# Performance work log

Hardware: AMD Instinct MI355X
Metric: run time of the kernel (lower is better)

## Reference

```python
import jax, jax.numpy as jnp
import numpy as np

H = 6      # n_attention_heads
BLK = 64


def adder1x1(x2d, w):
    """AdderNet 1x1 'convolution': Y[co, n] = -sum_ci |x2d[ci, n] - w[co, ci]|.
    Processed in output-channel blocks to bound the abs-diff intermediate.
    x2d: [Ci, N], w: [Co, Ci] -> [Co, N]
    """
    co, ci = w.shape
    wb = w.reshape(co // BLK, BLK, ci)
    def f(wblk):  # wblk: [BLK, Ci] -> [BLK, N]
        return -jnp.sum(jnp.abs(x2d[None, :, :] - wblk[:, :, None]), axis=1)
    return jax.lax.map(f, wb).reshape(co, -1)


def layernorm_all(y, w, b, eps=1e-5):
    # nn.LayerNorm([E, B, S]) applied to [1, E, B, S]: normalize over ALL of E,B,S
    mu = jnp.mean(y)
    var = jnp.mean((y - mu) ** 2)
    return (y - mu) * jax.lax.rsqrt(var + eps) * w + b


def layernorm_last(y, w, b, eps=1e-5):
    mu = jnp.mean(y, axis=-1, keepdims=True)
    var = jnp.mean((y - mu) ** 2, axis=-1, keepdims=True)
    return (y - mu) * jax.lax.rsqrt(var + eps) * w + b


def setup_inputs() -> dict:
    key = jax.random.key(0)
    ks = jax.random.split(key, 14)
    B, S, E = 8, 197, 384
    inp = {
        "x": jax.random.normal(ks[0], (B, S, E), jnp.float32),
        "wq": jax.random.normal(ks[1], (E, E), jnp.float32) * 0.05,
        "wk": jax.random.normal(ks[2], (E, E), jnp.float32) * 0.05,
        "wv": jax.random.normal(ks[3], (E, E), jnp.float32) * 0.05,
        "qln_w": 1.0 + 0.02 * jax.random.normal(ks[4], (E, B, S), jnp.float32),
        "qln_b": 0.02 * jax.random.normal(ks[5], (E, B, S), jnp.float32),
        "kln_w": 1.0 + 0.02 * jax.random.normal(ks[6], (E, B, S), jnp.float32),
        "kln_b": 0.02 * jax.random.normal(ks[7], (E, B, S), jnp.float32),
        "vln_w": 1.0 + 0.02 * jax.random.normal(ks[8], (E, B, S), jnp.float32),
        "vln_b": 0.02 * jax.random.normal(ks[9], (E, B, S), jnp.float32),
        "oln_w": 1.0 + 0.02 * jax.random.normal(ks[10], (E,), jnp.float32),
        "oln_b": 0.02 * jax.random.normal(ks[11], (E,), jnp.float32),
        "fc_w": jax.random.normal(ks[12], (E, E), jnp.float32) * 0.05,
        "fc_b": 0.02 * jax.random.normal(ks[13], (E,), jnp.float32),
    }
    return inp


def reference(x, wq, wk, wv, qln_w, qln_b, kln_w, kln_b, vln_w, vln_b,
              oln_w, oln_b, fc_w, fc_b):
    B, S, E = x.shape
    D = E // H
    scale = (2.0 * D * (1.0 - 2.0 / np.pi)) ** (-0.5)

    # torch: x.reshape(1, E, B, S) on contiguous [B,S,E] is a flat-buffer reshape
    x2d = x.reshape(E, B * S)  # [Ci, N]

    def proj(w, lw, lb):
        y = adder1x1(x2d, w).reshape(E, B, S)          # adder2d 1x1, bias=False
        y = layernorm_all(y, lw, lb)                    # LN over [E,B,S]
        y = y.reshape(B, S, H, D)                       # flat reshape (as torch)
        y = jnp.swapaxes(y, 1, 2)                       # [B,H,S,D]
        return y.reshape(B * H, S, D)

    q = proj(wq, qln_w, qln_b)
    k = proj(wk, kln_w, kln_b)
    v = proj(wv, vln_w, vln_b)

    att = jnp.einsum('bsd,btd->bst', q, k) * scale      # [B*H, S, S]
    att = jax.nn.softmax(att, axis=-1) + jnp.eye(S, dtype=x.dtype)
    o = jnp.einsum('bst,btd->bsd', att, v)              # [B*H, S, D]

    o = jnp.swapaxes(o.reshape(B, H, S, D), 1, 2).reshape(B, S, E)
    o = layernorm_last(o, oln_w, oln_b)
    return o @ fc_w.T + fc_b
```

## Files before the change

kernel.cpp:

```cpp
#include <hip/hip_runtime.h>
#include <math.h>

#ifndef M_PI
#define M_PI 3.14159265358979323846
#endif

#define B_ 8
#define S_ 197
#define E_ 384
#define H_ 6
#define D_ 64
#define N_ (B_*S_)
#define EN ((size_t)E_*N_)
#define NBLK_N 7
#define NBLK_ADD (NBLK_N*48)
#define NBLK_LN 591

__global__ __launch_bounds__(256) void k_adder(
    const float* __restrict__ x,
    const float* __restrict__ wq, const float* __restrict__ wk,
    const float* __restrict__ wv,
    float* __restrict__ Y, float* __restrict__ partials)
{
  const int p = blockIdx.z;
  const float* __restrict__ w = (p == 0) ? wq : (p == 1) ? wk : wv;
  const int co0 = blockIdx.y * 8;
  const int n = blockIdx.x * 256 + threadIdx.x;
  const bool nok = (n < N_);
  const int nc = nok ? n : 0;

  const float* __restrict__ xp = x + nc;
  const float* __restrict__ wp = w + (size_t)co0 * E_;

  float acc[8];
  #pragma unroll
  for (int r = 0; r < 8; ++r) acc[r] = 0.f;

  float xbA[8], xbB[8];
  #pragma unroll
  for (int k = 0; k < 8; ++k) xbA[k] = xp[(size_t)k * N_];

  #pragma unroll 1
  for (int c0 = 0; c0 < E_; c0 += 16) {
    #pragma unroll
    for (int k = 0; k < 8; ++k) xbB[k] = xp[(size_t)(c0 + 8 + k) * N_];
    #pragma unroll
    for (int r = 0; r < 8; ++r) {
      const float* wr = wp + (size_t)r * E_ + c0;
      #pragma unroll
      for (int k = 0; k < 8; ++k)
        acc[r] += fabsf(xbA[k] - wr[k]);
    }
    if (c0 + 16 < E_) {
      #pragma unroll
      for (int k = 0; k < 8; ++k) xbA[k] = xp[(size_t)(c0 + 16 + k) * N_];
    }
    #pragma unroll
    for (int r = 0; r < 8; ++r) {
      const float* wr = wp + (size_t)r * E_ + c0 + 8;
      #pragma unroll
      for (int k = 0; k < 8; ++k)
        acc[r] += fabsf(xbB[k] - wr[k]);
    }
  }

  float* Yp = Y + (size_t)p * EN;
  if (nok) {
    #pragma unroll
    for (int r = 0; r < 8; ++r)
      Yp[(size_t)(co0 + r) * N_ + n] = -acc[r];
  }

  float s1 = 0.f, s2 = 0.f;
  if (nok) {
    #pragma unroll
    for (int r = 0; r < 8; ++r) {
      s1 += -acc[r];
      s2 += acc[r] * acc[r];
    }
  }
  #pragma unroll
  for (int off = 32; off > 0; off >>= 1) {
    s1 += __shfl_down(s1, off);
    s2 += __shfl_down(s2, off);
  }
  __shared__ float red[8];
  const int tid = threadIdx.x;
  int wid = tid >> 6, lane = tid & 63;
  if (lane == 0) { red[wid * 2] = s1; red[wid * 2 + 1] = s2; }
  __syncthreads();
  if (tid == 0) {
    float t1 = red[0] + red[2] + red[4] + red[6];
    float t2 = red[1] + red[3] + red[5] + red[7];
    int blk = blockIdx.y * NBLK_N + blockIdx.x;
    partials[((size_t)p * NBLK_ADD + blk) * 2 + 0] = t1;
    partials[((size_t)p * NBLK_ADD + blk) * 2 + 1] = t2;
  }
}

__global__ __launch_bounds__(256) void k_stats(
    const float* __restrict__ partials, float* __restrict__ stats)
{
  const int p = blockIdx.x;
  const int tid = threadIdx.x;
  float s1 = 0.f, s2 = 0.f;
  for (int i = tid; i < NBLK_ADD; i += 256) {
    s1 += partials[((size_t)p * NBLK_ADD + i) * 2 + 0];
    s2 += partials[((size_t)p * NBLK_ADD + i) * 2 + 1];
  }
  #pragma unroll
  for (int off = 32; off > 0; off >>= 1) {
    s1 += __shfl_down(s1, off);
    s2 += __shfl_down(s2, off);
  }
  __shared__ float red[8];
  int wid = tid >> 6, lane = tid & 63;
  if (lane == 0) { red[wid * 2] = s1; red[wid * 2 + 1] = s2; }
  __syncthreads();
  if (tid == 0) {
    float S1 = red[0] + red[2] + red[4] + red[6];
    float S2 = red[1] + red[3] + red[5] + red[7];
    float mean = S1 / (float)EN;
    float var = S2 / (float)EN - mean * mean;
    stats[p * 2 + 0] = mean;
    stats[p * 2 + 1] = rsqrtf(var + 1e-5f);
  }
}

__global__ __launch_bounds__(256) void k_lnall(
    const float* __restrict__ Y, float* __restrict__ Z,
    const float* __restrict__ stats,
    const float* __restrict__ w0, const float* __restrict__ b0,
    const float* __restrict__ w1, const float* __restrict__ b1,
    const float* __restrict__ w2, const float* __restrict__ b2)
{
  const int p = blockIdx.y;
  const float* __restrict__ w = (p == 0) ? w0 : (p == 1) ? w1 : w2;
  const float* __restrict__ b = (p == 0) ? b0 : (p == 1) ? b1 : b2;
  const float mean = stats[p * 2 + 0];
  const float rstd = stats[p * 2 + 1];
  size_t i = ((size_t)blockIdx.x * 256 + threadIdx.x) * 4;
  const float* Yp = Y + (size_t)p * EN;
  float* Zp = Z + (size_t)p * EN;
  float4 y = *(const float4*)(Yp + i);
  float4 wv = *(const float4*)(w + i);
  float4 bv = *(const float4*)(b + i);
  float4 zv;
  zv.x = (y.x - mean) * rstd * wv.x + bv.x;
  zv.y = (y.y - mean) * rstd * wv.y + bv.y;
  zv.z = (y.z - mean) * rstd * wv.z + bv.z;
  zv.w = (y.w - mean) * rstd * wv.w + bv.w;
  *(float4*)(Zp + i) = zv;
}

__global__ __launch_bounds__(256) void k_attn(
    const float* __restrict__ zq, const float* __restrict__ zk,
    const float* __restrict__ zv, float* __restrict__ obuf, float scale)
{
  const int bh = blockIdx.x, b = bh / H_, h = bh % H_;
  const int s0 = blockIdx.y * 32;

  __shared__ float Qs[64][36];
  __shared__ float KVs[64][68];
  __shared__ float Ps[32][200];
  __shared__ float linv[32];

  const int tid = threadIdx.x;
  const int tx = tid & 15, ty = tid >> 4;

  #pragma unroll
  for (int it = 0; it < 2; ++it) {
    int idx = tid + it * 256;
    int sl = idx >> 4, c4 = (idx & 15) * 4;
    int s = s0 + sl;
    float4 v = make_float4(0.f, 0.f, 0.f, 0.f);
    if (s < S_) v = *(const float4*)(zq + (size_t)(b * S_ + s) * E_ + h * D_ + c4);
    Qs[c4 + 0][sl] = v.x; Qs[c4 + 1][sl] = v.y;
    Qs[c4 + 2][sl] = v.z; Qs[c4 + 3][sl] = v.w;
  }

  float accS[4][2][4];
  #pragma unroll
  for (int tt = 0; tt < 4; ++tt)
    #pragma unroll
    for (int r = 0; r < 2; ++r)
      #pragma unroll
      for (int j = 0; j < 4; ++j) accS[tt][r][j] = 0.f;

  #pragma unroll
  for (int tt = 0; tt < 4; ++tt) {
    __syncthreads();
    #pragma unroll
    for (int it = 0; it < 4; ++it) {
      int idx = tid + it * 256;
      int tl = idx >> 4, c4 = (idx & 15) * 4;
      int t = tt * 64 + tl;
      float4 u = make_float4(0.f, 0.f, 0.f, 0.f);
      if (t < S_) u = *(const float4*)(zk + (size_t)(b * S_ + t) * E_ + h * D_ + c4);
      KVs[c4 + 0][tl] = u.x; KVs[c4 + 1][tl] = u.y;
      KVs[c4 + 2][tl] = u.z; KVs[c4 + 3][tl] = u.w;
    }
    __syncthreads();
    #pragma unroll 8
    for (int d = 0; d < 64; ++d) {
      float2 q2 = *(const float2*)(&Qs[d][2 * ty]);
      float4 k4 = *(const float4*)(&KVs[d][tx * 4]);
      float ka[4] = {k4.x, k4.y, k4.z, k4.w};
      #pragma unroll
      for (int j = 0; j < 4; ++j) {
        accS[tt][0][j] += q2.x * ka[j];
        accS[tt][1][j] += q2.y * ka[j];
      }
    }
  }

  float mr0 = -1e30f, mr1 = -1e30f;
  #pragma unroll
  for (int tt = 0; tt < 4; ++tt)
    #pragma unroll
    for (int j = 0; j < 4; ++j) {
      int t = tt * 64 + tx * 4 + j;
      float v0 = (t < S_) ? accS[tt][0][j] * scale : -1e30f;
      float v1 = (t < S_) ? accS[tt][1][j] * scale : -1e30f;
      accS[tt][0][j] = v0; accS[tt][1][j] = v1;
      mr0 = fmaxf(mr0, v0); mr1 = fmaxf(mr1, v1);
    }
  #pragma unroll
  for (int off = 1; off < 16; off <<= 1) {
    mr0 = fmaxf(mr0, __shfl_xor(mr0, off));
    mr1 = fmaxf(mr1, __shfl_xor(mr1, off));
  }
  float sr0 = 0.f, sr1 = 0.f;
  #pragma unroll
  for (int tt = 0; tt < 4; ++tt)
    #pragma unroll
    for (int j = 0; j < 4; ++j) {
      float p0 = __expf(accS[tt][0][j] - mr0);
      float p1 = __expf(accS[tt][1][j] - mr1);
      accS[tt][0][j] = p0; accS[tt][1][j] = p1;
      sr0 += p0; sr1 += p1;
    }
  #pragma unroll
  for (int off = 1; off < 16; off <<= 1) {
    sr0 += __shfl_xor(sr0, off);
    sr1 += __shfl_xor(sr1, off);
  }
  if (tx == 0) { linv[2 * ty] = 1.f / sr0; linv[2 * ty + 1] = 1.f / sr1; }
  #pragma unroll
  for (int tt = 0; tt < 4; ++tt) {
    int t4 = tt * 64 + tx * 4;
    if (t4 < 200) {
      *(float4*)(&Ps[2 * ty][t4]) =
          make_float4(accS[tt][0][0], accS[tt][0][1], accS[tt][0][2], accS[tt][0][3]);
      *(float4*)(&Ps[2 * ty + 1][t4]) =
          make_float4(accS[tt][1][0], accS[tt][1][1], accS[tt][1][2], accS[tt][1][3]);
    }
  }

  float accO[2][4];
  #pragma unroll
  for (int r = 0; r < 2; ++r)
    #pragma unroll
    for (int j = 0; j < 4; ++j) accO[r][j] = 0.f;

  #pragma unroll
  for (int tt = 0; tt < 4; ++tt) {
    __syncthreads();
    #pragma unroll
    for (int it = 0; it < 4; ++it) {
      int idx = tid + it * 256;
      int tl = idx >> 4, c4 = (idx & 15) * 4;
      int t = tt * 64 + tl;
      float4 u = make_float4(0.f, 0.f, 0.f, 0.f);
      if (t < S_) u = *(const float4*)(zv + (size_t)(b * S_ + t) * E_ + h * D_ + c4);
      *(float4*)(&KVs[tl][c4]) = u;
    }
    __syncthreads();
    const int tmax = (tt < 3) ? 64 : 8;
    #pragma unroll 8
    for (int tl = 0; tl < tmax; ++tl) {
      float p0 = Ps[2 * ty][tt * 64 + tl];
      float p1 = Ps[2 * ty + 1][tt * 64 + tl];
      float4 v4 = *(const float4*)(&KVs[tl][tx * 4]);
      float va[4] = {v4.x, v4.y, v4.z, v4.w};
      #pragma unroll
      for (int j = 0; j < 4; ++j) {
        accO[0][j] += p0 * va[j];
        accO[1][j] += p1 * va[j];
      }
    }
  }

  #pragma unroll
  for (int r = 0; r < 2; ++r) {
    int s = s0 + 2 * ty + r;
    if (s < S_) {
      float inv = linv[2 * ty + r];
      float4 vs = *(const float4*)(zv + (size_t)(b * S_ + s) * E_ + h * D_ + tx * 4);
      float4 o;
      o.x = accO[r][0] * inv + vs.x;
      o.y = accO[r][1] * inv + vs.y;
      o.z = accO[r][2] * inv + vs.z;
      o.w = accO[r][3] * inv + vs.w;
      *(float4*)(obuf + (size_t)(b * S_ + s) * E_ + h * D_ + tx * 4) = o;
    }
  }
}

__global__ __launch_bounds__(256) void k_lnlast(
    const float* __restrict__ obuf,
    const float* __restrict__ lw, const float* __restrict__ lb,
    float* __restrict__ oln)
{
  const int row = blockIdx.x * 4 + (threadIdx.x >> 6);
  const int lane = threadIdx.x & 63;
  const float* base = obuf + (size_t)row * E_;
  float v[6];
  float s1 = 0.f;
  #pragma unroll
  for (int j = 0; j < 6; ++j) { v[j] = base[lane + 64 * j]; s1 += v[j]; }
  #pragma unroll
  for (int off = 32; off > 0; off >>= 1) s1 += __shfl_xor(s1, off);
  float mean = s1 * (1.f / E_);
  float s2 = 0.f;
  #pragma unroll
  for (int j = 0; j < 6; ++j) { float d = v[j] - mean; s2 += d * d; }
  #pragma unroll
  for (int off = 32; off > 0; off >>= 1) s2 += __shfl_xor(s2, off);
  float rstd = rsqrtf(s2 * (1.f / E_) + 1e-5f);
  float* ob = oln + (size_t)row * E_;
  #pragma unroll
  for (int j = 0; j < 6; ++j) {
    int e = lane + 64 * j;
    ob[e] = (v[j] - mean) * rstd * lw[e] + lb[e];
  }
}

__global__ __launch_bounds__(256) void k_fc(
    const float* __restrict__ oln, const float* __restrict__ fcw,
    const float* __restrict__ fcb, float* __restrict__ out)
{
  const int j0 = blockIdx.x * 64, n0 = blockIdx.y * 32;
  __shared__ float Xs[16][36];
  __shared__ float Ws[16][68];
  const int tid = threadIdx.x;
  const int tx = tid & 15, ty = tid >> 4;
  float acc[4][2];
  #pragma unroll
  for (int i = 0; i < 4; ++i) { acc[i][0] = 0.f; acc[i][1] = 0.f; }

  for (int e0 = 0; e0 < E_; e0 += 16) {
    {
      int nl = tid >> 3, e2 = (tid & 7) * 2;
      int n = n0 + nl;
      float2 v = make_float2(0.f, 0.f);
      if (n < N_) v = *(const float2*)(oln + (size_t)n * E_ + e0 + e2);
      Xs[e2 + 0][nl] = v.x; Xs[e2 + 1][nl] = v.y;
      int jl = tid >> 2, c4 = (tid & 3) * 4;
      float4 u = *(const float4*)(fcw + (size_t)(j0 + jl) * E_ + e0 + c4);
      Ws[c4 + 0][jl] = u.x; Ws[c4 + 1][jl] = u.y;
      Ws[c4 + 2][jl] = u.z; Ws[c4 + 3][jl] = u.w;
    }
    __syncthreads();
    #pragma unroll
    for (int cc = 0; cc < 16; ++cc) {
      float2 x2 = *(const float2*)(&Xs[cc][tx * 2]);
      float4 w4 = *(const float4*)(&Ws[cc][ty * 4]);
      float xa[2] = {x2.x, x2.y};
      float wa[4] = {w4.x, w4.y, w4.z, w4.w};
      #pragma unroll
      for (int i = 0; i < 4; ++i) {
        acc[i][0] += wa[i] * xa[0];
        acc[i][1] += wa[i] * xa[1];
      }
    }
    __syncthreads();
  }
  const int jc = j0 + ty * 4;
  float4 bv = *(const float4*)(fcb + jc);
  #pragma unroll
  for (int jn = 0; jn < 2; ++jn) {
    int n = n0 + tx * 2 + jn;
    if (n < N_) {
      float4 o;
      o.x = acc[0][jn] + bv.x;
      o.y = acc[1][jn] + bv.y;
      o.z = acc[2][jn] + bv.z;
      o.w = acc[3][jn] + bv.w;
      *(float4*)(out + (size_t)n * E_ + jc) = o;
    }
  }
}

extern "C" void kernel_launch(void* const* d_in, const int* in_sizes, int n_in,
                              void* d_out, int out_size, void* d_ws, size_t ws_size,
                              hipStream_t stream)
{
  const float* x   = (const float*)d_in[0];
  const float* wq  = (const float*)d_in[1];
  const float* wk  = (const float*)d_in[2];
  const float* wv  = (const float*)d_in[3];
  const float* qw  = (const float*)d_in[4];
  const float* qb  = (const float*)d_in[5];
  const float* kw  = (const float*)d_in[6];
  const float* kb  = (const float*)d_in[7];
  const float* vw  = (const float*)d_in[8];
  const float* vb  = (const float*)d_in[9];
  const float* ow  = (const float*)d_in[10];
  const float* obp = (const float*)d_in[11];
  const float* fcw = (const float*)d_in[12];
  const float* fcb = (const float*)d_in[13];
  float* out = (float*)d_out;
  float* ws  = (float*)d_ws;

  float* Y     = ws;
  float* Z     = ws + 3 * EN;
  float* obuf  = ws + 0 * EN;
  float* oln   = ws + 1 * EN;
  float* part  = ws + 6 * EN;
  float* stats = part + 3 * NBLK_ADD * 2;

  const float scale = (float)pow(2.0 * D_ * (1.0 - 2.0 / M_PI), -0.5);

  k_adder<<<dim3(NBLK_N, 48, 3), 256, 0, stream>>>(x, wq, wk, wv, Y, part);
  k_stats<<<dim3(3), 256, 0, stream>>>(part, stats);
  k_lnall<<<dim3(NBLK_LN, 3), 256, 0, stream>>>(Y, Z, stats, qw, qb, kw, kb, vw, vb);
  const float* zq = Z;
  const float* zk = Z + EN;
  const float* zv = Z + 2 * EN;
  k_attn<<<dim3(48, 7), 256, 0, stream>>>(zq, zk, zv, obuf, scale);
  k_lnlast<<<dim3(394), 256, 0, stream>>>(obuf, ow, obp, oln);
  k_fc<<<dim3(6, 50), 256, 0, stream>>>(oln, fcw, fcb, out);
}
```

Baseline: 117.6 us.

## Shrink per-block tiles in adder and attention kernels to raise block counts

The adder kernel now has each block compute 6 output channels instead of 8, so the grid's y dimension grows from 48 to 64. Its x-row prefetch goes from two to four 8-wide register buffers per 32-channel step. The attention kernel now gives each block 16 query rows instead of 32, with one row per thread group, raising its grid from 7 to 13 blocks per head, and Q is stored row-major in shared memory. The aim is more blocks for better occupancy and load balance across CUs, at the cost of reloading K/V tiles for twice as many attention blocks and more x-buffer registers in the adder.

```diff
diff --git a/kernel.cpp b/kernel.cpp
--- a/kernel.cpp
+++ b/kernel.cpp
@@ -13,7 +13,8 @@
 #define N_ (B_*S_)
 #define EN ((size_t)E_*N_)
 #define NBLK_N 7
-#define NBLK_ADD (NBLK_N*48)
+#define NBLK_CO 64
+#define NBLK_ADD (NBLK_N*NBLK_CO)
 #define NBLK_LN 591
 
 __global__ __launch_bounds__(256) void k_adder(
@@ -24,7 +25,7 @@
 {
   const int p = blockIdx.z;
   const float* __restrict__ w = (p == 0) ? wq : (p == 1) ? wk : wv;
-  const int co0 = blockIdx.y * 8;
+  const int co0 = blockIdx.y * 6;
   const int n = blockIdx.x * 256 + threadIdx.x;
   const bool nok = (n < N_);
   const int nc = nok ? n : 0;
@@ -32,49 +33,75 @@
   const float* __restrict__ xp = x + nc;
   const float* __restrict__ wp = w + (size_t)co0 * E_;
 
-  float acc[8];
-  #pragma unroll
-  for (int r = 0; r < 8; ++r) acc[r] = 0.f;
-
-  float xbA[8], xbB[8];
-  #pragma unroll
-  for (int k = 0; k < 8; ++k) xbA[k] = xp[(size_t)k * N_];
+  float acc[6];
+  #pragma unroll
+  for (int r = 0; r < 6; ++r) acc[r] = 0.f;
+
+  float xb0[8], xb1[8], xb2[8], xb3[8];
+  #pragma unroll
+  for (int k = 0; k < 8; ++k) {
+    xb0[k] = xp[(size_t)(k +  0) * N_];
+    xb1[k] = xp[(size_t)(k +  8) * N_];
+    xb2[k] = xp[(size_t)(k + 16) * N_];
+    xb3[k] = xp[(size_t)(k + 24) * N_];
+  }
 
   #pragma unroll 1
-  for (int c0 = 0; c0 < E_; c0 += 16) {
-    #pragma unroll
-    for (int k = 0; k < 8; ++k) xbB[k] = xp[(size_t)(c0 + 8 + k) * N_];
-    #pragma unroll
-    for (int r = 0; r < 8; ++r) {
+  for (int c0 = 0; c0 < E_; c0 += 32) {
+    const bool more = (c0 + 32) < E_;
+    #pragma unroll
+    for (int r = 0; r < 6; ++r) {
       const float* wr = wp + (size_t)r * E_ + c0;
       #pragma unroll
-      for (int k = 0; k < 8; ++k)
-        acc[r] += fabsf(xbA[k] - wr[k]);
-    }
-    if (c0 + 16 < E_) {
-      #pragma unroll
-      for (int k = 0; k < 8; ++k) xbA[k] = xp[(size_t)(c0 + 16 + k) * N_];
-    }
-    #pragma unroll
-    for (int r = 0; r < 8; ++r) {
+      for (int k = 0; k < 8; ++k) acc[r] += fabsf(xb0[k] - wr[k]);
+    }
+    if (more) {
+      #pragma unroll
+      for (int k = 0; k < 8; ++k) xb0[k] = xp[(size_t)(c0 + 32 + k) * N_];
+    }
+    #pragma unroll
+    for (int r = 0; r < 6; ++r) {
       const float* wr = wp + (size_t)r * E_ + c0 + 8;
       #pragma unroll
-      for (int k = 0; k < 8; ++k)
-        acc[r] += fabsf(xbB[k] - wr[k]);
+      for (int k = 0; k < 8; ++k) acc[r] += fabsf(xb1[k] - wr[k]);
+    }
+    if (more) {
+      #pragma unroll
+      for (int k = 0; k < 8; ++k) xb1[k] = xp[(size_t)(c0 + 40 + k) * N_];
+    }
+    #pragma unroll
+    for (int r = 0; r < 6; ++r) {
+      const float* wr = wp + (size_t)r * E_ + c0 + 16;
+      #pragma unroll
+      for (int k = 0; k < 8; ++k) acc[r] += fabsf(xb2[k] - wr[k]);
+    }
+    if (more) {
+      #pragma unroll
+      for (int k = 0; k < 8; ++k) xb2[k] = xp[(size_t)(c0 + 48 + k) * N_];
+    }
+    #pragma unroll
+    for (int r = 0; r < 6; ++r) {
+      const float* wr = wp + (size_t)r * E_ + c0 + 24;
+      #pragma unroll
+      for (int k = 0; k < 8; ++k) acc[r] += fabsf(xb3[k] - wr[k]);
+    }
+    if (more) {
+      #pragma unroll
+      for (int k = 0; k < 8; ++k) xb3[k] = xp[(size_t)(c0 + 56 + k) * N_];
     }
   }
 
   float* Yp = Y + (size_t)p * EN;
   if (nok) {
     #pragma unroll
-    for (int r = 0; r < 8; ++r)
+    for (int r = 0; r < 6; ++r)
       Yp[(size_t)(co0 + r) * N_ + n] = -acc[r];
   }
 
   float s1 = 0.f, s2 = 0.f;
   if (nok) {
     #pragma unroll
-    for (int r = 0; r < 8; ++r) {
+    for (int r = 0; r < 6; ++r) {
       s1 += -acc[r];
       s2 += acc[r] * acc[r];
     }
@@ -158,34 +185,30 @@
     const float* __restrict__ zv, float* __restrict__ obuf, float scale)
 {
   const int bh = blockIdx.x, b = bh / H_, h = bh % H_;
-  const int s0 = blockIdx.y * 32;
-
-  __shared__ float Qs[64][36];
+  const int s0 = blockIdx.y * 16;
+
+  __shared__ float Qs[16][68];
   __shared__ float KVs[64][68];
-  __shared__ float Ps[32][200];
-  __shared__ float linv[32];
+  __shared__ float Ps[16][200];
+  __shared__ float linv[16];
 
   const int tid = threadIdx.x;
-  const int tx = tid & 15, ty = tid >> 4;
-
-  #pragma unroll
-  for (int it = 0; it < 2; ++it) {
-    int idx = tid + it * 256;
-    int sl = idx >> 4, c4 = (idx & 15) * 4;
+  const int tx = tid & 15;
+  const int ty = tid >> 4;
+
+  {
+    int sl = tid >> 4, c4 = (tid & 15) * 4;
     int s = s0 + sl;
     float4 v = make_float4(0.f, 0.f, 0.f, 0.f);
     if (s < S_) v = *(const float4*)(zq + (size_t)(b * S_ + s) * E_ + h * D_ + c4);
-    Qs[c4 + 0][sl] = v.x; Qs[c4 + 1][sl] = v.y;
-    Qs[c4 + 2][sl] = v.z; Qs[c4 + 3][sl] = v.w;
-  }
-
-  float accS[4][2][4];
+    *(float4*)(&Qs[sl][c4]) = v;
+  }
+
+  float accS[4][4];
   #pragma unroll
   for (int tt = 0; tt < 4; ++tt)
     #pragma unroll
-    for (int r = 0; r < 2; ++r)
-      #pragma unroll
-      for (int j = 0; j < 4; ++j) accS[tt][r][j] = 0.f;
+    for (int j = 0; j < 4; ++j) accS[tt][j] = 0.f;
 
   #pragma unroll
   for (int tt = 0; tt < 4; ++tt) {
@@ -201,68 +224,54 @@
       KVs[c4 + 2][tl] = u.z; KVs[c4 + 3][tl] = u.w;
     }
     __syncthreads();
-    #pragma unroll 8
-    for (int d = 0; d < 64; ++d) {
-      float2 q2 = *(const float2*)(&Qs[d][2 * ty]);
-      float4 k4 = *(const float4*)(&KVs[d][tx * 4]);
-      float ka[4] = {k4.x, k4.y, k4.z, k4.w};
-      #pragma unroll
-      for (int j = 0; j < 4; ++j) {
-        accS[tt][0][j] += q2.x * ka[j];
-        accS[tt][1][j] += q2.y * ka[j];
+    #pragma unroll 4
+    for (int dd = 0; dd < 16; ++dd) {
+      float4 q4 = *(const float4*)(&Qs[ty][dd * 4]);
+      float qa[4] = {q4.x, q4.y, q4.z, q4.w};
+      #pragma unroll
+      for (int k = 0; k < 4; ++k) {
+        float4 k4 = *(const float4*)(&KVs[dd * 4 + k][tx * 4]);
+        accS[tt][0] += qa[k] * k4.x;
+        accS[tt][1] += qa[k] * k4.y;
+        accS[tt][2] += qa[k] * k4.z;
+        accS[tt][3] += qa[k] * k4.w;
       }
     }
   }
 
-  float mr0 = -1e30f, mr1 = -1e30f;
+  float m = -1e30f;
   #pragma unroll
   for (int tt = 0; tt < 4; ++tt)
     #pragma unroll
     for (int j = 0; j < 4; ++j) {
       int t = tt * 64 + tx * 4 + j;
-      float v0 = (t < S_) ? accS[tt][0][j] * scale : -1e30f;
-      float v1 = (t < S_) ? accS[tt][1][j] * scale : -1e30f;
-      accS[tt][0][j] = v0; accS[tt][1][j] = v1;
-      mr0 = fmaxf(mr0, v0); mr1 = fmaxf(mr1, v1);
-    }
-  #pragma unroll
-  for (int off = 1; off < 16; off <<= 1) {
-    mr0 = fmaxf(mr0, __shfl_xor(mr0, off));
-    mr1 = fmaxf(mr1, __shfl_xor(mr1, off));
-  }
-  float sr0 = 0.f, sr1 = 0.f;
+      float v = (t < S_) ? accS[tt][j] * scale : -1e30f;
+      accS[tt][j] = v;
+      m = fmaxf(m, v);
+    }
+  #pragma unroll
+  for (int off = 1; off < 16; off <<= 1) m = fmaxf(m, __shfl_xor(m, off));
+  float sum = 0.f;
   #pragma unroll
   for (int tt = 0; tt < 4; ++tt)
     #pragma unroll
     for (int j = 0; j < 4; ++j) {
-      float p0 = __expf(accS[tt][0][j] - mr0);
-      float p1 = __expf(accS[tt][1][j] - mr1);
-      accS[tt][0][j] = p0; accS[tt][1][j] = p1;
-      sr0 += p0; sr1 += p1;
-    }
-  #pragma unroll
-  for (int off = 1; off < 16; off <<= 1) {
-    sr0 += __shfl_xor(sr0, off);
-    sr1 += __shfl_xor(sr1, off);
-  }
-  if (tx == 0) { linv[2 * ty] = 1.f / sr0; linv[2 * ty + 1] = 1.f / sr1; }
+      float pv = __expf(accS[tt][j] - m);
+      accS[tt][j] = pv;
+      sum += pv;
+    }
+  #pragma unroll
+  for (int off = 1; off < 16; off <<= 1) sum += __shfl_xor(sum, off);
+  if (tx == 0) linv[ty] = 1.f / sum;
   #pragma unroll
   for (int tt = 0; tt < 4; ++tt) {
     int t4 = tt * 64 + tx * 4;
-    if (t4 < 200) {
-      *(float4*)(&Ps[2 * ty][t4]) =
-          make_float4(accS[tt][0][0], accS[tt][0][1], accS[tt][0][2], accS[tt][0][3]);
-      *(float4*)(&Ps[2 * ty + 1][t4]) =
-          make_float4(accS[tt][1][0], accS[tt][1][1], accS[tt][1][2], accS[tt][1][3]);
-    }
-  }
-
-  float accO[2][4];
-  #pragma unroll
-  for (int r = 0; r < 2; ++r)
-    #pragma unroll
-    for (int j = 0; j < 4; ++j) accO[r][j] = 0.f;
-
+    if (t4 < 200)
+      *(float4*)(&Ps[ty][t4]) =
+          make_float4(accS[tt][0], accS[tt][1], accS[tt][2], accS[tt][3]);
+  }
+
+  float accO[4] = {0.f, 0.f, 0.f, 0.f};
   #pragma unroll
   for (int tt = 0; tt < 4; ++tt) {
     __syncthreads();
@@ -279,31 +288,25 @@
     const int tmax = (tt < 3) ? 64 : 8;
     #pragma unroll 8
     for (int tl = 0; tl < tmax; ++tl) {
-      float p0 = Ps[2 * ty][tt * 64 + tl];
-      float p1 = Ps[2 * ty + 1][tt * 64 + tl];
+      float pp = Ps[ty][tt * 64 + tl];
       float4 v4 = *(const float4*)(&KVs[tl][tx * 4]);
-      float va[4] = {v4.x, v4.y, v4.z, v4.w};
-      #pragma unroll
-      for (int j = 0; j < 4; ++j) {
-        accO[0][j] += p0 * va[j];
-        accO[1][j] += p1 * va[j];
-      }
-    }
-  }
-
-  #pragma unroll
-  for (int r = 0; r < 2; ++r) {
-    int s = s0 + 2 * ty + r;
-    if (s < S_) {
-      float inv = linv[2 * ty + r];
-      float4 vs = *(const float4*)(zv + (size_t)(b * S_ + s) * E_ + h * D_ + tx * 4);
-      float4 o;
-      o.x = accO[r][0] * inv + vs.x;
-      o.y = accO[r][1] * inv + vs.y;
-      o.z = accO[r][2] * inv + vs.z;
-      o.w = accO[r][3] * inv + vs.w;
-      *(float4*)(obuf + (size_t)(b * S_ + s) * E_ + h * D_ + tx * 4) = o;
-    }
+      accO[0] += pp * v4.x;
+      accO[1] += pp * v4.y;
+      accO[2] += pp * v4.z;
+      accO[3] += pp * v4.w;
+    }
+  }
+
+  const int s = s0 + ty;
+  if (s < S_) {
+    float inv = linv[ty];
+    float4 vs = *(const float4*)(zv + (size_t)(b * S_ + s) * E_ + h * D_ + tx * 4);
+    float4 o;
+    o.x = accO[0] * inv + vs.x;
+    o.y = accO[1] * inv + vs.y;
+    o.z = accO[2] * inv + vs.z;
+    o.w = accO[3] * inv + vs.w;
+    *(float4*)(obuf + (size_t)(b * S_ + s) * E_ + h * D_ + tx * 4) = o;
   }
 }
 
@@ -422,13 +425,13 @@
 
   const float scale = (float)pow(2.0 * D_ * (1.0 - 2.0 / M_PI), -0.5);
 
-  k_adder<<<dim3(NBLK_N, 48, 3), 256, 0, stream>>>(x, wq, wk, wv, Y, part);
+  k_adder<<<dim3(NBLK_N, NBLK_CO, 3), 256, 0, stream>>>(x, wq, wk, wv, Y, part);
   k_stats<<<dim3(3), 256, 0, stream>>>(part, stats);
   k_lnall<<<dim3(NBLK_LN, 3), 256, 0, stream>>>(Y, Z, stats, qw, qb, kw, kb, vw, vb);
   const float* zq = Z;
   const float* zk = Z + EN;
   const float* zv = Z + 2 * EN;
-  k_attn<<<dim3(48, 7), 256, 0, stream>>>(zq, zk, zv, obuf, scale);
+  k_attn<<<dim3(48, 13), 256, 0, stream>>>(zq, zk, zv, obuf, scale);
   k_lnlast<<<dim3(394), 256, 0, stream>>>(obuf, ow, obp, oln);
   k_fc<<<dim3(6, 50), 256, 0, stream>>>(oln, fcw, fcb, out);
 }
```

New measurement: 167.4 us. 1.42x slower.
